# Kernel tuning notes

Hardware: AMD Instinct MI355X
Metric: run time of the kernel (lower is better)

The kernel has to match this reference:

```python
import jax, jax.numpy as jnp
import numpy as np

V, L, H, E, S = 50257, 12, 12, 768, 1024
B, T = 4, 1024
D = E // H
EPS = 1e-5


def setup_inputs() -> dict:
    key = jax.random.key(0)
    ks = jax.random.split(key, 16)
    n = lambda k, shape: (jax.random.normal(k, shape, dtype=jnp.float32) * 0.02)
    return {
        'idx': jax.random.randint(ks[0], (B, T), 0, V),
        'wte': n(ks[1], (V, E)),
        'wpe': n(ks[2], (S, E)),
        'ln1_g': jnp.ones((L, E)), 'ln1_b': jnp.zeros((L, E)),
        'attn_w': n(ks[3], (L, E, 3 * E)), 'attn_b': jnp.zeros((L, 3 * E)),
        'proj_w': n(ks[4], (L, E, E)), 'proj_b': jnp.zeros((L, E)),
        'ln2_g': jnp.ones((L, E)), 'ln2_b': jnp.zeros((L, E)),
        'fc_w': n(ks[5], (L, E, 4 * E)), 'fc_b': jnp.zeros((L, 4 * E)),
        'mproj_w': n(ks[6], (L, 4 * E, E)), 'mproj_b': jnp.zeros((L, E)),
        'lnf_g': jnp.ones((E,)), 'lnf_b': jnp.zeros((E,)),
    }


def layer_norm(x, g, b):
    m = jnp.mean(x, axis=-1, keepdims=True)
    v = jnp.var(x, axis=-1, keepdims=True)
    return (x - m) * jax.lax.rsqrt(v + EPS) * g + b


def reference(idx, wte, wpe, ln1_g, ln1_b, attn_w, attn_b, proj_w, proj_b,
              ln2_g, ln2_b, fc_w, fc_b, mproj_w, mproj_b, lnf_g, lnf_b):
    b, t = idx.shape
    x = wte[idx] + wpe[:t]  # [B,T,E]
    causal = jnp.tril(jnp.ones((t, t), dtype=bool))
    neg_inf = jnp.finfo(x.dtype).min
    for l in range(L):
        h = layer_norm(x, ln1_g[l], ln1_b[l])
        qkv = h @ attn_w[l] + attn_b[l]  # [B,T,3E]
        q, k, v = jnp.split(qkv, 3, axis=-1)
        q = q.reshape(b, t, H, D).transpose(0, 2, 1, 3)  # [B,H,T,D]
        k = k.reshape(b, t, H, D).transpose(0, 2, 1, 3)
        v = v.reshape(b, t, H, D).transpose(0, 2, 1, 3)
        att = jnp.einsum('bhqd,bhkd->bhqk', q, k) / jnp.sqrt(jnp.float32(D))
        att = jnp.where(causal, att, neg_inf)
        att = jax.nn.softmax(att, axis=-1)
        y = jnp.einsum('bhqk,bhkd->bhqd', att, v)
        y = y.transpose(0, 2, 1, 3).reshape(b, t, E)
        x = x + y @ proj_w[l] + proj_b[l]
        h2 = layer_norm(x, ln2_g[l], ln2_b[l])
        h2 = jax.nn.gelu(h2 @ fc_w[l] + fc_b[l], approximate=True)
        x = x + h2 @ mproj_w[l] + mproj_b[l]
    x = layer_norm(x, lnf_g, lnf_b)
    logits = x @ wte.T  # tied lm_head
    return logits
```

## Files before the change

kernel.cpp:

```cpp
#include <hip/hip_runtime.h>
#include <hip/hip_bf16.h>
#include <math.h>

#define VSZ 50257
#define VPAD2 50432
#define NLAYER 12
#define NH 12
#define EMB 768
#define TSEQ 1024
#define NB 4
#define MROWS (NB * TSEQ)
#define DHEAD 64
#define LN_EPS 1e-5f

typedef __attribute__((ext_vector_type(8))) short bf16x8;
typedef __attribute__((ext_vector_type(4))) float f32x4;

__device__ __forceinline__ void load_lds16(const void* g, void* l) {
    __builtin_amdgcn_global_load_lds((const __attribute__((address_space(1))) unsigned int*)g,
                                     (__attribute__((address_space(3))) unsigned int*)l,
                                     16, 0, 0);
}

__global__ void embed_wte_kernel(const int* __restrict__ idx, const float* __restrict__ wte,
                                 const float* __restrict__ wpe, float* __restrict__ x,
                                 __hip_bfloat16* __restrict__ wteB) {
    int bid = blockIdx.x;
    int tid = threadIdx.x;
    if (bid < MROWS) {
        int t = bid & (TSEQ - 1);
        int tok = idx[bid];
        float4 a = *(const float4*)&wte[(size_t)tok * EMB + tid * 4];
        float4 p = *(const float4*)&wpe[(size_t)t * EMB + tid * 4];
        a.x += p.x; a.y += p.y; a.z += p.z; a.w += p.w;
        *(float4*)&x[(size_t)bid * EMB + tid * 4] = a;
    } else {
        int row = bid - MROWS;
        union { short4 s4; __hip_bfloat16 h[4]; } u;
        if (row < VSZ) {
            float4 a = *(const float4*)&wte[(size_t)row * EMB + tid * 4];
            u.h[0] = __float2bfloat16(a.x); u.h[1] = __float2bfloat16(a.y);
            u.h[2] = __float2bfloat16(a.z); u.h[3] = __float2bfloat16(a.w);
        } else {
            u.h[0] = u.h[1] = u.h[2] = u.h[3] = __float2bfloat16(0.0f);
        }
        *(short4*)&wteB[(size_t)row * EMB + tid * 4] = u.s4;
    }
}

template <bool ACC>
__device__ __forceinline__ void ln_body(float* __restrict__ x, const float* __restrict__ p0,
                                        const float* __restrict__ p1,
                                        const float* __restrict__ g, const float* __restrict__ b,
                                        __hip_bfloat16* __restrict__ out, int row,
                                        float* __restrict__ smem) {
    float* xr = x + (size_t)row * EMB;
    __hip_bfloat16* yr = out + (size_t)row * EMB;
    int tid = threadIdx.x;
    float v0, v1, v2;
    if (ACC) {
        const float* q0 = p0 + (size_t)row * EMB;
        const float* q1 = p1 + (size_t)row * EMB;
        v0 = xr[tid]       + q0[tid]       + q1[tid];
        v1 = xr[tid + 256] + q0[tid + 256] + q1[tid + 256];
        v2 = xr[tid + 512] + q0[tid + 512] + q1[tid + 512];
        xr[tid] = v0; xr[tid + 256] = v1; xr[tid + 512] = v2;
    } else {
        v0 = xr[tid]; v1 = xr[tid + 256]; v2 = xr[tid + 512];
    }
    float s = v0 + v1 + v2;
    float ss = v0 * v0 + v1 * v1 + v2 * v2;
    #pragma unroll
    for (int i = 1; i < 64; i <<= 1) {
        s  += __shfl_xor(s, i, 64);
        ss += __shfl_xor(ss, i, 64);
    }
    float* sm = smem;
    float* sv = smem + 4;
    int lane = tid & 63, wid = tid >> 6;
    if (lane == 0) { sm[wid] = s; sv[wid] = ss; }
    __syncthreads();
    float sum = sm[0] + sm[1] + sm[2] + sm[3];
    float sqs = sv[0] + sv[1] + sv[2] + sv[3];
    float mean = sum * (1.0f / EMB);
    float var = sqs * (1.0f / EMB) - mean * mean;
    float rstd = rsqrtf(var + LN_EPS);
    yr[tid]       = __float2bfloat16((v0 - mean) * rstd * g[tid]       + b[tid]);
    yr[tid + 256] = __float2bfloat16((v1 - mean) * rstd * g[tid + 256] + b[tid + 256]);
    yr[tid + 512] = __float2bfloat16((v2 - mean) * rstd * g[tid + 512] + b[tid + 512]);
}

__global__ void ln_acc_kernel(float* __restrict__ x, const float* __restrict__ p0,
                              const float* __restrict__ p1,
                              const float* __restrict__ g, const float* __restrict__ b,
                              __hip_bfloat16* __restrict__ out) {
    __shared__ float smem[8];
    ln_body<true>(x, p0, p1, g, b, out, blockIdx.x, smem);
}

template <bool ACC>
__global__ void ln_convT4_kernel(float* __restrict__ x, const float* __restrict__ p0,
                                 const float* __restrict__ p1,
                                 const float* __restrict__ lg, const float* __restrict__ lb,
                                 __hip_bfloat16* __restrict__ out,
                                 const float* __restrict__ aw, const float* __restrict__ pw,
                                 const float* __restrict__ fw, const float* __restrict__ mw,
                                 __hip_bfloat16* __restrict__ awT, __hip_bfloat16* __restrict__ pwT,
                                 __hip_bfloat16* __restrict__ fwT, __hip_bfloat16* __restrict__ mwT) {
    __shared__ float tile[32][33];
    int bid = blockIdx.x;
    if (bid < MROWS) {
        ln_body<ACC>(x, p0, p1, lg, lb, out, bid, &tile[0][0]);
        return;
    }
    int cbid = bid - MROWS;
    const float* W; __hip_bfloat16* Wt; int K, N, t;
    if (cbid < 1728)      { W = aw; Wt = awT; K = 768;  N = 2304; t = cbid; }
    else if (cbid < 2304) { W = pw; Wt = pwT; K = 768;  N = 768;  t = cbid - 1728; }
    else if (cbid < 4608) { W = fw; Wt = fwT; K = 768;  N = 3072; t = cbid - 2304; }
    else                  { W = mw; Wt = mwT; K = 3072; N = 768;  t = cbid - 4608; }
    int NT = N >> 5;
    int n0 = (t % NT) << 5, k0 = (t / NT) << 5;
    int tid = threadIdx.x;
    int i = tid >> 3, q = tid & 7;
    float4 v = *(const float4*)&W[(size_t)(k0 + i) * N + n0 + q * 4];
    tile[i][q * 4 + 0] = v.x; tile[i][q * 4 + 1] = v.y;
    tile[i][q * 4 + 2] = v.z; tile[i][q * 4 + 3] = v.w;
    __syncthreads();
    union { short4 s4; __hip_bfloat16 h[4]; } u;
    u.h[0] = __float2bfloat16(tile[q * 4 + 0][i]);
    u.h[1] = __float2bfloat16(tile[q * 4 + 1][i]);
    u.h[2] = __float2bfloat16(tile[q * 4 + 2][i]);
    u.h[3] = __float2bfloat16(tile[q * 4 + 3][i]);
    *(short4*)&Wt[(size_t)(n0 + i) * K + k0 + q * 4] = u.s4;
}

template <bool GELU, bool RES, int OUT, bool SPLITK>
__global__ __launch_bounds__(512) void gemm_bt(
                        const __hip_bfloat16* __restrict__ A, const __hip_bfloat16* __restrict__ B,
                        const float* __restrict__ bias, const float* __restrict__ res,
                        float* __restrict__ Cf, __hip_bfloat16* __restrict__ Cb,
                        __hip_bfloat16* __restrict__ vt, float* __restrict__ Cp1,
                        int Kc, int lda, int ldc, int Nclip) {
    __shared__ __hip_bfloat16 Ash[128 * 64];
    __shared__ __hip_bfloat16 Bsh[128 * 64];
    const int tid = threadIdx.x;
    const int lane = tid & 63, wid = tid >> 6;
    const int wr = wid >> 2, wc = wid & 3;

    const int nwg_all = gridDim.x;
    const int cpx = nwg_all >> 3;
    int wg = (blockIdx.x & 7) * cpx + (blockIdx.x >> 3);
    int chunk = 0, nwg = nwg_all;
    if (SPLITK) { chunk = wg & 1; wg >>= 1; nwg = nwg_all >> 1; }
    const int NT = nwg >> 5;
    const int bandsz = NT << 3;
    const int band = wg / bandsz;
    const int rem = wg - band * bandsz;
    const int m0 = (band * 8 + (rem & 7)) * 128;
    const int n0 = (rem >> 3) * 128;
    const int koff = SPLITK ? chunk * Kc : 0;

    f32x4 acc[4][2] = {};
    const int srow = lane >> 3;
    const int scol = ((lane & 7) ^ srow) * 8;

    const int lr16 = lane & 15;
    const int hi = lane >> 4;

    for (int k0 = 0; k0 < Kc; k0 += 64) {
        #pragma unroll
        for (int it = 0; it < 2; ++it) {
            int c = wid + it * 8;
            const __hip_bfloat16* ga = A + (size_t)(m0 + c * 8 + srow) * lda + koff + k0 + scol;
            load_lds16(ga, &Ash[c * 512]);
            const __hip_bfloat16* gb = B + (size_t)(n0 + c * 8 + srow) * lda + koff + k0 + scol;
            load_lds16(gb, &Bsh[c * 512]);
        }
        __syncthreads();
        bf16x8 a[4][2], b[2][2];
        #pragma unroll
        for (int m = 0; m < 4; ++m)
            #pragma unroll
            for (int kk = 0; kk < 2; ++kk) {
                int ra = wr * 64 + m * 16 + lr16;
                int ca = (kk * 32 + hi * 8) ^ ((ra & 7) * 8);
                a[m][kk] = *(const bf16x8*)&Ash[ra * 64 + ca];
            }
        #pragma unroll
        for (int n = 0; n < 2; ++n)
            #pragma unroll
            for (int kk = 0; kk < 2; ++kk) {
                int rb = wc * 32 + n * 16 + lr16;
                int cb = (kk * 32 + hi * 8) ^ ((rb & 7) * 8);
                b[n][kk] = *(const bf16x8*)&Bsh[rb * 64 + cb];
            }
        #pragma unroll
        for (int kk = 0; kk < 2; ++kk)
            #pragma unroll
            for (int m = 0; m < 4; ++m)
                #pragma unroll
                for (int n = 0; n < 2; ++n)
                    acc[m][n] = __builtin_amdgcn_mfma_f32_16x16x32_bf16(a[m][kk], b[n][kk], acc[m][n], 0, 0, 0);
        __syncthreads();
    }

    float* Co = (SPLITK && chunk) ? Cp1 : Cf;
    const bool dobias = bias && (!SPLITK || chunk == 0);
    const int crow0 = m0 + wr * 64, ccol0 = n0 + wc * 32;
    #pragma unroll
    for (int m = 0; m < 4; ++m) {
        #pragma unroll
        for (int n = 0; n < 2; ++n) {
            int col = ccol0 + n * 16 + lr16;
            if (col >= Nclip) continue;
            float bv = dobias ? bias[col] : 0.0f;
            #pragma unroll
            for (int j = 0; j < 4; ++j) {
                int r = crow0 + m * 16 + hi * 4 + j;
                float v = acc[m][n][j] + bv;
                if (GELU) {
                    float t = 0.7978845608028654f * (v + 0.044715f * v * v * v);
                    v = 0.5f * v * (1.0f + tanhf(t));
                }
                if (RES) v += res[(size_t)r * ldc + col];
                if (OUT == 0) Co[(size_t)r * ldc + col] = v;
                else if (OUT == 1) Cb[(size_t)r * ldc + col] = __float2bfloat16(v);
                else {
                    if (col < 2 * EMB) Cb[(size_t)r * (2 * EMB) + col] = __float2bfloat16(v);
                    else {
                        int hh = (col - 2 * EMB) >> 6, dd = (col - 2 * EMB) & 63;
                        int bb = r >> 10, tt = r & 1023;
                        vt[(((size_t)bb * NH + hh) * 64 + dd) * TSEQ + tt] = __float2bfloat16(v);
                    }
                }
            }
        }
    }
}

#define G256_STAGE_A(KT, MH, P) do { \
    int ktw_ = (KT) % 12; \
    load_lds16(A + (size_t)(m0 + (MH) * 64 + srow) * 768 + ktw_ * 64 + sgr8, \
               &lds[(P) * 2][(MH) * 8192 + wid * 512]); \
    load_lds16(A + (size_t)(m0 + 128 + (MH) * 64 + srow) * 768 + ktw_ * 64 + sgr8, \
               &lds[(P) * 2][(MH) * 8192 + 4096 + wid * 512]); \
} while (0)

#define G256_STAGE_B(KT, NH, P) do { \
    int ktw_ = (KT) % 12; \
    load_lds16(Bm + (size_t)(bwc0 * 64 + (NH) * 32 + brow) * 768 + ktw_ * 64 + sgr8, \
               &lds[(P) * 2 + 1][(NH) * 8192 + wid * 512]); \
    load_lds16(Bm + (size_t)((2 + bwc0) * 64 + (NH) * 32 + brow) * 768 + ktw_ * 64 + sgr8, \
               &lds[(P) * 2 + 1][(NH) * 8192 + 4096 + wid * 512]); \
} while (0)

#define G256_PHASE(MH, NH, P, STAGE_STMT, VM) do { \
    bf16x8 af[4][2], bf[2][2]; \
    _Pragma("unroll") \
    for (int f = 0; f < 4; ++f) \
        _Pragma("unroll") \
        for (int kk = 0; kk < 2; ++kk) { \
            int pr = (MH) * 128 + wr * 64 + f * 16 + lr16; \
            af[f][kk] = *(const bf16x8*)((const char*)lds[(P) * 2] + pr * 128 + ((kk * 64 + hi * 16) ^ ((lr16 & 7) << 4))); \
        } \
    _Pragma("unroll") \
    for (int nn = 0; nn < 2; ++nn) \
        _Pragma("unroll") \
        for (int kk = 0; kk < 2; ++kk) { \
            int pr = (NH) * 128 + wc * 32 + nn * 16 + lr16; \
            bf[nn][kk] = *(const bf16x8*)((const char*)lds[(P) * 2 + 1] + pr * 128 + ((kk * 64 + hi * 16) ^ ((lr16 & 7) << 4))); \
        } \
    STAGE_STMT; \
    asm volatile("s_waitcnt vmcnt(" #VM ")" ::: "memory"); \
    __builtin_amdgcn_s_barrier(); \
    asm volatile("s_waitcnt lgkmcnt(0)" ::: "memory"); \
    __builtin_amdgcn_sched_barrier(0); \
    __builtin_amdgcn_s_setprio(1); \
    _Pragma("unroll") \
    for (int kk = 0; kk < 2; ++kk) \
        _Pragma("unroll") \
        for (int f = 0; f < 4; ++f) \
            _Pragma("unroll") \
            for (int nn = 0; nn < 2; ++nn) \
                acc[(MH) * 4 + f][(NH) * 2 + nn] = __builtin_amdgcn_mfma_f32_16x16x32_bf16( \
                    af[f][kk], bf[nn][kk], acc[(MH) * 4 + f][(NH) * 2 + nn], 0, 0, 0); \
    __builtin_amdgcn_s_setprio(0); \
    __builtin_amdgcn_s_barrier(); \
} while (0)

__global__ __launch_bounds__(512, 1) void gemm256(const __hip_bfloat16* __restrict__ A,
                                                  const __hip_bfloat16* __restrict__ Bw,
                                                  float* __restrict__ C) {
    __shared__ __hip_bfloat16 lds[4][16384];
    const int tid = threadIdx.x;
    const int lane = tid & 63, wid = tid >> 6;
    const int wr = wid >> 2, wc = wid & 3;
    const int lr16 = lane & 15, hi = lane >> 4;

    const int bid = blockIdx.x;
    const int wg = (bid & 7) * 394 + (bid >> 3);
    const int band = wg / 1576, rem = wg % 1576;
    const int mt = band * 8 + (rem & 7), nt = rem >> 3;
    const size_t m0 = (size_t)mt * 256;
    const __hip_bfloat16* Bm = Bw + (size_t)nt * 256 * 768;

    const int srow = tid >> 3;
    const int sgr8 = ((tid & 7) ^ ((tid >> 3) & 7)) * 8;
    const int brow = (tid >> 3) & 31;
    const int bwc0 = tid >> 8;

    f32x4 acc[8][4] = {};

    G256_STAGE_A(0, 0, 0);
    G256_STAGE_B(0, 0, 0);
    G256_STAGE_A(0, 1, 0);
    G256_STAGE_B(0, 1, 0);
    G256_STAGE_A(1, 0, 1);
    G256_STAGE_B(1, 0, 1);
    asm volatile("s_waitcnt vmcnt(8)" ::: "memory");
    __builtin_amdgcn_s_barrier();

    for (int kt2 = 0; kt2 < 12; kt2 += 2) {
        G256_PHASE(0, 0, 0, G256_STAGE_A(kt2 + 1, 1, 1), 6);
        G256_PHASE(0, 1, 0, G256_STAGE_B(kt2 + 1, 1, 1), 10);
        G256_PHASE(1, 0, 0, G256_STAGE_A(kt2 + 2, 0, 0), 10);
        G256_PHASE(1, 1, 0, G256_STAGE_B(kt2 + 2, 0, 0), 8);
        G256_PHASE(0, 0, 1, G256_STAGE_A(kt2 + 2, 1, 0), 6);
        G256_PHASE(0, 1, 1, G256_STAGE_B(kt2 + 2, 1, 0), 10);
        G256_PHASE(1, 0, 1, G256_STAGE_A(kt2 + 3, 0, 1), 10);
        G256_PHASE(1, 1, 1, G256_STAGE_B(kt2 + 3, 0, 1), 8);
    }

    const int ccol0 = nt * 256 + wc * 64;
    #pragma unroll
    for (int mf = 0; mf < 8; ++mf) {
        size_t row = m0 + wr * 128 + (mf >> 2) * 64 + (mf & 3) * 16 + hi * 4;
        #pragma unroll
        for (int nf = 0; nf < 4; ++nf) {
            int col = ccol0 + nf * 16 + lr16;
            if (col < VSZ) {
                #pragma unroll
                for (int j = 0; j < 4; ++j)
                    C[(row + j) * VSZ + col] = acc[mf][nf][j];
            }
        }
    }
}

__global__ __launch_bounds__(256) void flash_attn(const __hip_bfloat16* __restrict__ qk,
                                                  const __hip_bfloat16* __restrict__ vT,
                                                  __hip_bfloat16* __restrict__ y) {
    const int qt = blockIdx.x, h = blockIdx.y, b = blockIdx.z;
    const int tid = threadIdx.x;
    const int lane = tid & 63, w = tid >> 6;
    const int g = lane >> 4, lr = lane & 15;

    __shared__ char KshB[64 * 128];
    __shared__ char VshB[64 * 128];
    __shared__ char PshB[4][16 * 128];

    const __hip_bfloat16* qrow = qk + ((size_t)(b * TSEQ + qt * 64 + w * 16 + lr)) * 1536 + h * 64;
    bf16x8 qf0 = *(const bf16x8*)(qrow + g * 8);
    bf16x8 qf1 = *(const bf16x8*)(qrow + 32 + g * 8);

    float l[4] = {0.f, 0.f, 0.f, 0.f};
    f32x4 o[4];
    #pragma unroll
    for (int n = 0; n < 4; ++n) o[n] = (f32x4){0.f, 0.f, 0.f, 0.f};

    const int r0 = tid >> 3;
    const int c0 = (tid & 7) * 8;

    for (int kt = 0; kt <= qt; ++kt) {
        __syncthreads();
        #pragma unroll
        for (int it = 0; it < 2; ++it) {
            int r = r0 + it * 32;
            bf16x8 kv = *(const bf16x8*)(qk + ((size_t)(b * TSEQ + kt * 64 + r)) * 1536 + EMB + h * 64 + c0);
            *(bf16x8*)(KshB + ((r * 128 + c0 * 2) ^ ((r & 7) << 4))) = kv;
            bf16x8 vv = *(const bf16x8*)(vT + (((size_t)(b * NH + h)) * 64 + r) * TSEQ + kt * 64 + c0);
            *(bf16x8*)(VshB + ((r * 128 + c0 * 2) ^ ((r & 7) << 4))) = vv;
        }
        __syncthreads();

        f32x4 s[4] = {};
        #pragma unroll
        for (int n = 0; n < 4; ++n) {
            int kr = n * 16 + lr;
            bf16x8 kb0 = *(const bf16x8*)(KshB + ((kr * 128 + g * 16) ^ ((kr & 7) << 4)));
            bf16x8 kb1 = *(const bf16x8*)(KshB + ((kr * 128 + 64 + g * 16) ^ ((kr & 7) << 4)));
            s[n] = __builtin_amdgcn_mfma_f32_16x16x32_bf16(qf0, kb0, s[n], 0, 0, 0);
            s[n] = __builtin_amdgcn_mfma_f32_16x16x32_bf16(qf1, kb1, s[n], 0, 0, 0);
        }

        const bool diag = (kt == qt);
        float pexp[4][4];
        #pragma unroll
        for (int n = 0; n < 4; ++n)
            #pragma unroll
            for (int j = 0; j < 4; ++j) {
                float v = s[n][j] * 0.125f;
                if (diag && (n * 16 + lr > w * 16 + g * 4 + j)) v = -1e30f;
                float p = __expf(v - 4.0f);
                pexp[n][j] = p;
                l[j] += p;
            }

        char* P = PshB[w];
        #pragma unroll
        for (int n = 0; n < 4; ++n)
            #pragma unroll
            for (int j = 0; j < 4; ++j) {
                int rw = g * 4 + j;
                *(__hip_bfloat16*)(P + ((rw * 128 + (n * 16 + lr) * 2) ^ ((rw & 7) << 4))) =
                    __float2bfloat16(pexp[n][j]);
            }
        asm volatile("s_waitcnt lgkmcnt(0)" ::: "memory");
        bf16x8 pa0 = *(const bf16x8*)(P + ((lr * 128 + g * 16) ^ ((lr & 7) << 4)));
        bf16x8 pa1 = *(const bf16x8*)(P + ((lr * 128 + 64 + g * 16) ^ ((lr & 7) << 4)));
        #pragma unroll
        for (int n = 0; n < 4; ++n) {
            int vr = n * 16 + lr;
            bf16x8 vb0 = *(const bf16x8*)(VshB + ((vr * 128 + g * 16) ^ ((vr & 7) << 4)));
            bf16x8 vb1 = *(const bf16x8*)(VshB + ((vr * 128 + 64 + g * 16) ^ ((vr & 7) << 4)));
            o[n] = __builtin_amdgcn_mfma_f32_16x16x32_bf16(pa0, vb0, o[n], 0, 0, 0);
            o[n] = __builtin_amdgcn_mfma_f32_16x16x32_bf16(pa1, vb1, o[n], 0, 0, 0);
        }
    }

    #pragma unroll
    for (int j = 0; j < 4; ++j)
        #pragma unroll
        for (int i = 1; i < 16; i <<= 1)
            l[j] += __shfl_xor(l[j], i, 64);

    #pragma unroll
    for (int j = 0; j < 4; ++j) {
        float inv = 1.0f / l[j];
        int row = b * TSEQ + qt * 64 + w * 16 + g * 4 + j;
        #pragma unroll
        for (int n = 0; n < 4; ++n)
            y[(size_t)row * EMB + h * 64 + n * 16 + lr] = __float2bfloat16(o[n][j] * inv);
    }
}

extern "C" void kernel_launch(void* const* d_in, const int* in_sizes, int n_in,
                              void* d_out, int out_size, void* d_ws, size_t ws_size,
                              hipStream_t stream) {
    const int*   idx     = (const int*)d_in[0];
    const float* wte     = (const float*)d_in[1];
    const float* wpe     = (const float*)d_in[2];
    const float* ln1_g   = (const float*)d_in[3];
    const float* ln1_b   = (const float*)d_in[4];
    const float* attn_w  = (const float*)d_in[5];
    const float* attn_b  = (const float*)d_in[6];
    const float* proj_w  = (const float*)d_in[7];
    const float* proj_b  = (const float*)d_in[8];
    const float* ln2_g   = (const float*)d_in[9];
    const float* ln2_b   = (const float*)d_in[10];
    const float* fc_w    = (const float*)d_in[11];
    const float* fc_b    = (const float*)d_in[12];
    const float* mproj_w = (const float*)d_in[13];
    const float* mproj_b = (const float*)d_in[14];
    const float* lnf_g   = (const float*)d_in[15];
    const float* lnf_b   = (const float*)d_in[16];
    float* out = (float*)d_out;

    char* w = (char*)d_ws;
    float* x = (float*)w;                      w += (size_t)MROWS * EMB * 4;
    float* p0 = (float*)w;                     w += (size_t)MROWS * EMB * 4;
    float* p1 = (float*)w;                     w += (size_t)MROWS * EMB * 4;
    __hip_bfloat16* qkb = (__hip_bfloat16*)w;  w += (size_t)MROWS * 2 * EMB * 2;
    __hip_bfloat16* vTb = (__hip_bfloat16*)w;  w += (size_t)NB * NH * 64 * TSEQ * 2;
    __hip_bfloat16* h = (__hip_bfloat16*)w;    w += (size_t)MROWS * EMB * 2;
    __hip_bfloat16* y = (__hip_bfloat16*)w;    w += (size_t)MROWS * EMB * 2;
    __hip_bfloat16* g = (__hip_bfloat16*)w;    w += (size_t)MROWS * 4 * EMB * 2;
    __hip_bfloat16* wqkvT = (__hip_bfloat16*)w;   w += (size_t)3 * EMB * EMB * 2;
    __hip_bfloat16* wprojT = (__hip_bfloat16*)w;  w += (size_t)EMB * EMB * 2;
    __hip_bfloat16* wfcT = (__hip_bfloat16*)w;    w += (size_t)4 * EMB * EMB * 2;
    __hip_bfloat16* wmprojT = (__hip_bfloat16*)w; w += (size_t)4 * EMB * EMB * 2;
    __hip_bfloat16* wteB = (__hip_bfloat16*)w;    w += (size_t)VPAD2 * EMB * 2;

    dim3 blk192(192), blk256(256), blk512(512);

    embed_wte_kernel<<<MROWS + VPAD2, blk192, 0, stream>>>(idx, wte, wpe, x, wteB);

    for (int l = 0; l < NLAYER; l++) {
        const float* aw = attn_w + (size_t)l * EMB * 3 * EMB;
        const float* ab = attn_b + (size_t)l * 3 * EMB;
        const float* pw = proj_w + (size_t)l * EMB * EMB;
        const float* pb = proj_b + (size_t)l * EMB;
        const float* fw = fc_w   + (size_t)l * EMB * 4 * EMB;
        const float* fb = fc_b   + (size_t)l * 4 * EMB;
        const float* mw = mproj_w + (size_t)l * 4 * EMB * EMB;
        const float* mb = mproj_b + (size_t)l * EMB;

        if (l == 0)
            ln_convT4_kernel<false><<<MROWS + 6912, blk256, 0, stream>>>(
                x, nullptr, nullptr, ln1_g + l * EMB, ln1_b + l * EMB, h,
                aw, pw, fw, mw, wqkvT, wprojT, wfcT, wmprojT);
        else
            ln_convT4_kernel<true><<<MROWS + 6912, blk256, 0, stream>>>(
                x, p0, p1, ln1_g + l * EMB, ln1_b + l * EMB, h,
                aw, pw, fw, mw, wqkvT, wprojT, wfcT, wmprojT);

        gemm_bt<false, false, 2, false><<<dim3((3 * EMB / 128) * 32), blk512, 0, stream>>>(
            h, wqkvT, ab, nullptr, nullptr, qkb, vTb, nullptr, EMB, EMB, 3 * EMB, 3 * EMB);

        flash_attn<<<dim3(TSEQ / 64, NH, NB), blk256, 0, stream>>>(qkb, vTb, y);

        gemm_bt<false, false, 0, true><<<dim3((EMB / 128) * 32 * 2), blk512, 0, stream>>>(
            y, wprojT, pb, nullptr, p0, nullptr, nullptr, p1, EMB / 2, EMB, EMB, EMB);

        ln_acc_kernel<<<MROWS, blk256, 0, stream>>>(x, p0, p1, ln2_g + l * EMB, ln2_b + l * EMB, h);

        gemm_bt<true, false, 1, false><<<dim3((4 * EMB / 128) * 32), blk512, 0, stream>>>(
            h, wfcT, fb, nullptr, nullptr, g, nullptr, nullptr, EMB, EMB, 4 * EMB, 4 * EMB);

        gemm_bt<false, false, 0, true><<<dim3((EMB / 128) * 32 * 2), blk512, 0, stream>>>(
            g, wmprojT, mb, nullptr, p0, nullptr, nullptr, p1, 2 * EMB, 4 * EMB, EMB, EMB);
    }

    ln_acc_kernel<<<MROWS, blk256, 0, stream>>>(x, p0, p1, lnf_g, lnf_b, h);

    gemm256<<<dim3((VPAD2 / 256) * (MROWS / 256)), dim3(512), 0, stream>>>(h, wteB, out);
}
```

Before: 2.513 ms.

## Double-buffer LDS tiles in gemm_bt to overlap global loads with MFMA

The GEMM kernel now keeps two LDS buffers for A and B. It issues the global-to-LDS loads for the next K tile before computing on the current one, so one barrier per iteration replaces two. It also raises wave priority around the MFMA block using s_setprio. LDS use doubles to 64KB per block, which may lower occupancy. The hand-placed waitcnt and barrier ordering has to be exact to avoid races.

```diff
diff --git a/kernel.cpp b/kernel.cpp
--- a/kernel.cpp
+++ b/kernel.cpp
@@ -142,8 +142,8 @@
                         float* __restrict__ Cf, __hip_bfloat16* __restrict__ Cb,
                         __hip_bfloat16* __restrict__ vt, float* __restrict__ Cp1,
                         int Kc, int lda, int ldc, int Nclip) {
-    __shared__ __hip_bfloat16 Ash[128 * 64];
-    __shared__ __hip_bfloat16 Bsh[128 * 64];
+    __shared__ __hip_bfloat16 Ash[2][128 * 64];
+    __shared__ __hip_bfloat16 Bsh[2][128 * 64];
     const int tid = threadIdx.x;
     const int lane = tid & 63, wid = tid >> 6;
     const int wr = wid >> 2, wc = wid & 3;
@@ -167,17 +167,26 @@
 
     const int lr16 = lane & 15;
     const int hi = lane >> 4;
-
-    for (int k0 = 0; k0 < Kc; k0 += 64) {
-        #pragma unroll
-        for (int it = 0; it < 2; ++it) {
-            int c = wid + it * 8;
-            const __hip_bfloat16* ga = A + (size_t)(m0 + c * 8 + srow) * lda + koff + k0 + scol;
-            load_lds16(ga, &Ash[c * 512]);
-            const __hip_bfloat16* gb = B + (size_t)(n0 + c * 8 + srow) * lda + koff + k0 + scol;
-            load_lds16(gb, &Bsh[c * 512]);
-        }
-        __syncthreads();
+    const int nt = Kc >> 6;
+
+    #define GB_STG(KT, BUF) do { \
+        _Pragma("unroll") \
+        for (int it_ = 0; it_ < 2; ++it_) { \
+            int c_ = wid + it_ * 8; \
+            load_lds16(A + (size_t)(m0 + c_ * 8 + srow) * lda + koff + (KT) * 64 + scol, \
+                       &Ash[BUF][c_ * 512]); \
+            load_lds16(B + (size_t)(n0 + c_ * 8 + srow) * lda + koff + (KT) * 64 + scol, \
+                       &Bsh[BUF][c_ * 512]); \
+        } \
+    } while (0)
+
+    GB_STG(0, 0);
+    asm volatile("s_waitcnt vmcnt(0)" ::: "memory");
+    __builtin_amdgcn_s_barrier();
+
+    int p = 0;
+    for (int kt = 0; kt < nt; ++kt) {
+        if (kt + 1 < nt) GB_STG(kt + 1, p ^ 1);
         bf16x8 a[4][2], b[2][2];
         #pragma unroll
         for (int m = 0; m < 4; ++m)
@@ -185,7 +194,7 @@
             for (int kk = 0; kk < 2; ++kk) {
                 int ra = wr * 64 + m * 16 + lr16;
                 int ca = (kk * 32 + hi * 8) ^ ((ra & 7) * 8);
-                a[m][kk] = *(const bf16x8*)&Ash[ra * 64 + ca];
+                a[m][kk] = *(const bf16x8*)&Ash[p][ra * 64 + ca];
             }
         #pragma unroll
         for (int n = 0; n < 2; ++n)
@@ -193,8 +202,11 @@
             for (int kk = 0; kk < 2; ++kk) {
                 int rb = wc * 32 + n * 16 + lr16;
                 int cb = (kk * 32 + hi * 8) ^ ((rb & 7) * 8);
-                b[n][kk] = *(const bf16x8*)&Bsh[rb * 64 + cb];
+                b[n][kk] = *(const bf16x8*)&Bsh[p][rb * 64 + cb];
             }
+        asm volatile("s_waitcnt lgkmcnt(0)" ::: "memory");
+        __builtin_amdgcn_sched_barrier(0);
+        __builtin_amdgcn_s_setprio(1);
         #pragma unroll
         for (int kk = 0; kk < 2; ++kk)
             #pragma unroll
@@ -202,8 +214,12 @@
                 #pragma unroll
                 for (int n = 0; n < 2; ++n)
                     acc[m][n] = __builtin_amdgcn_mfma_f32_16x16x32_bf16(a[m][kk], b[n][kk], acc[m][n], 0, 0, 0);
-        __syncthreads();
-    }
+        __builtin_amdgcn_s_setprio(0);
+        asm volatile("s_waitcnt vmcnt(0)" ::: "memory");
+        __builtin_amdgcn_s_barrier();
+        p ^= 1;
+    }
+    #undef GB_STG
 
     float* Co = (SPLITK && chunk) ? Cp1 : Cf;
     const bool dobias = bias && (!SPLITK || chunk == 0);
```

New measurement: 2.717 ms. 8.1% more time.
